# Performance work log

Hardware: AMD Instinct MI355X
Metric: run time of the kernel (lower is better)

Reference implementation:

```python
import jax, jax.numpy as jnp
import numpy as np

N = 50000      # nodes
D = 16         # regular in/out degree
E = N * D      # edges
IN_N = 128     # input node feature size
IN_E = 64      # input edge feature size
H = 64         # internal_size
H2 = 2 * H     # LSTM input/hidden size
OUT_N = 128
OUT_E = 64


def setup_inputs() -> dict:
    key = jax.random.key(0)
    ks = jax.random.split(key, 24)
    s = 0.05
    inp = {}
    inp["node_vecs"] = jax.random.normal(ks[0], (N, IN_N), jnp.float32)
    inp["edge_vecs"] = jax.random.normal(ks[1], (E, IN_E), jnp.float32)
    # ring digraph: edge e = i*D + k connects i -> (i+k+1) % N
    j = np.arange(N)[:, None]
    k = np.arange(D)[None, :]
    pni = (j - (k + 1)) % N
    inp["pred_node_idx"] = jnp.asarray(pni, jnp.int32)
    inp["pred_edge_idx"] = jnp.asarray(pni * D + k, jnp.int32)
    inp["succ_node_idx"] = jnp.asarray((j + k + 1) % N, jnp.int32)
    inp["succ_edge_idx"] = jnp.asarray(j * D + k, jnp.int32)
    src = np.repeat(np.arange(N), D)
    dst = (src + np.tile(np.arange(1, D + 1), N)) % N
    inp["edge_src"] = jnp.asarray(src, jnp.int32)
    inp["edge_dst"] = jnp.asarray(dst, jnp.int32)
    # parameters (torch Linear convention: y = x @ W.T + b)
    inp["Wn"] = jax.random.normal(ks[2], (H, IN_N), jnp.float32) * s
    inp["bn"] = jax.random.normal(ks[3], (H,), jnp.float32) * s
    inp["We"] = jax.random.normal(ks[4], (H, IN_E), jnp.float32) * s
    inp["be"] = jax.random.normal(ks[5], (H,), jnp.float32) * s
    # two LSTM aggregators (pred / succ), gate order i,f,g,o
    inp["Wih_p"] = jax.random.normal(ks[6], (4 * H2, H2), jnp.float32) * s
    inp["Whh_p"] = jax.random.normal(ks[7], (4 * H2, H2), jnp.float32) * s
    inp["bih_p"] = jax.random.normal(ks[8], (4 * H2,), jnp.float32) * s
    inp["bhh_p"] = jax.random.normal(ks[9], (4 * H2,), jnp.float32) * s
    inp["Wr_p"] = jax.random.normal(ks[10], (H, H2), jnp.float32) * s
    inp["br_p"] = jax.random.normal(ks[11], (H,), jnp.float32) * s
    inp["Wih_s"] = jax.random.normal(ks[12], (4 * H2, H2), jnp.float32) * s
    inp["Whh_s"] = jax.random.normal(ks[13], (4 * H2, H2), jnp.float32) * s
    inp["bih_s"] = jax.random.normal(ks[14], (4 * H2,), jnp.float32) * s
    inp["bhh_s"] = jax.random.normal(ks[15], (4 * H2,), jnp.float32) * s
    inp["Wr_s"] = jax.random.normal(ks[16], (H, H2), jnp.float32) * s
    inp["br_s"] = jax.random.normal(ks[17], (H,), jnp.float32) * s
    inp["Wt_n"] = jax.random.normal(ks[18], (OUT_N, 3 * H), jnp.float32) * s
    inp["bt_n"] = jax.random.normal(ks[19], (OUT_N,), jnp.float32) * s
    inp["Wt_e"] = jax.random.normal(ks[20], (OUT_E, 3 * H), jnp.float32) * s
    inp["bt_e"] = jax.random.normal(ks[21], (OUT_E,), jnp.float32) * s
    return inp


def _lstm_last(seq, Wih, Whh, bih, bhh):
    # seq: [N, D, 2H] -> last-timestep hidden state [N, 2H]
    n = seq.shape[0]
    h0 = jnp.zeros((n, H2), seq.dtype)

    def step(carry, x):
        h, c = carry
        g = x @ Wih.T + h @ Whh.T + (bih + bhh)
        i, f, gg, o = jnp.split(g, 4, axis=-1)
        c = jax.nn.sigmoid(f) * c + jax.nn.sigmoid(i) * jnp.tanh(gg)
        h = jax.nn.sigmoid(o) * jnp.tanh(c)
        return (h, c), None

    (h, _), _ = jax.lax.scan(step, (h0, h0), jnp.swapaxes(seq, 0, 1))
    return h


def _aggregate(hN, hE, nidx, eidx, Wih, Whh, bih, bhh, Wr, br):
    # gather neighbor sequences: concat(node pretrans, edge pretrans) -> [N, D, 2H]
    seq = jnp.concatenate([hN[nidx], hE[eidx]], axis=-1)
    h_last = _lstm_last(seq, Wih, Whh, bih, bhh)
    return jax.nn.relu(jax.nn.relu(h_last) @ Wr.T + br)  # [N, H]


def reference(node_vecs, edge_vecs, pred_node_idx, pred_edge_idx,
              succ_node_idx, succ_edge_idx, edge_src, edge_dst,
              Wn, bn, We, be,
              Wih_p, Whh_p, bih_p, bhh_p, Wr_p, br_p,
              Wih_s, Whh_s, bih_s, bhh_s, Wr_s, br_s,
              Wt_n, bt_n, Wt_e, bt_e):
    hN = jax.nn.relu(node_vecs @ Wn.T + bn)   # [N, H] node pretrans
    hE = jax.nn.relu(edge_vecs @ We.T + be)   # [E, H] edge pretrans
    agg_p = _aggregate(hN, hE, pred_node_idx, pred_edge_idx,
                       Wih_p, Whh_p, bih_p, bhh_p, Wr_p, br_p)
    agg_s = _aggregate(hN, hE, succ_node_idx, succ_edge_idx,
                       Wih_s, Whh_s, bih_s, bhh_s, Wr_s, br_s)
    node_in = jnp.concatenate([agg_p, hN, agg_s], axis=-1)      # [N, 3H]
    node_out = jax.nn.relu(node_in @ Wt_n.T + bt_n)             # [N, OUT_N]
    edge_in = jnp.concatenate([hN[edge_src], hE, hN[edge_dst]], axis=-1)  # [E, 3H]
    edge_out = jax.nn.relu(edge_in @ Wt_e.T + bt_e)             # [E, OUT_E]
    return node_out, edge_out
```

## Files before the change

### kernel.cpp

```cpp
#include <hip/hip_runtime.h>

#define DEV __device__ __forceinline__

typedef __bf16 bf16x8 __attribute__((ext_vector_type(8)));
typedef float floatx4 __attribute__((ext_vector_type(4)));
typedef unsigned short u16;

constexpr int NN    = 50000;
constexpr int DEG   = 16;
constexpr int H2    = 128;

constexpr size_t WS_WN    = 0;
constexpr size_t WS_WE    = 16384;
constexpr size_t WS_WIH_P = 24576;
constexpr size_t WS_WHH_P = 155648;
constexpr size_t WS_WR_P  = 286720;
constexpr size_t WS_WIH_S = 303104;
constexpr size_t WS_WHH_S = 434176;
constexpr size_t WS_WR_S  = 565248;
constexpr size_t WS_WT_N  = 581632;
constexpr size_t WS_WT_E  = 630784;
constexpr size_t WS_BSUM_P= 655360;
constexpr size_t WS_BSUM_S= 657408;
constexpr size_t WS_HN    = 659456;
constexpr size_t WS_AGGP  = 7059456;
constexpr size_t WS_AGGS  = 13459456;

DEV u16 f2bf(float x) {
  unsigned u = __builtin_bit_cast(unsigned, x);
  return (u16)((u + 0x7fffu + ((u >> 16) & 1u)) >> 16);
}
DEV bf16x8 ld8(const u16* p) { return *reinterpret_cast<const bf16x8*>(p); }
DEV floatx4 mfma16(bf16x8 a, bf16x8 b, floatx4 c) {
  return __builtin_amdgcn_mfma_f32_16x16x32_bf16(a, b, c, 0, 0, 0);
}
DEV floatx4 make4(float b) { floatx4 r = {b, b, b, b}; return r; }
DEV float sigf(float x) { return __builtin_amdgcn_rcpf(1.0f + __expf(-x)); }
DEV float expc(float x) { return __expf(fminf(x, 60.0f)); }
DEV bf16x8 relu8(bf16x8 a) {
  typedef u16 u16x8 __attribute__((ext_vector_type(8)));
  u16x8 u = __builtin_bit_cast(u16x8, a);
#pragma unroll
  for (int i = 0; i < 8; ++i) u[i] = (u[i] & 0x8000u) ? (u16)0 : u[i];
  return __builtin_bit_cast(bf16x8, u);
}

__global__ void k_prep(const float* Wn, const float* We,
                       const float* WihP, const float* WhhP, const float* WrP,
                       const float* WihS, const float* WhhS, const float* WrS,
                       const float* WtN, const float* WtE,
                       const float* bihP, const float* bhhP,
                       const float* bihS, const float* bhhS,
                       u16* wbf, float* bsumP, float* bsumS) {
  int idx = blockIdx.x * blockDim.x + threadIdx.x;
  if (idx < 327680) {
    const float* src; int rel;
    if      (idx <   8192) { src = Wn;   rel = idx; }
    else if (idx <  12288) { src = We;   rel = idx - 8192; }
    else if (idx <  77824) { src = WihP; rel = idx - 12288; }
    else if (idx < 143360) { src = WhhP; rel = idx - 77824; }
    else if (idx < 151552) { src = WrP;  rel = idx - 143360; }
    else if (idx < 217088) { src = WihS; rel = idx - 151552; }
    else if (idx < 282624) { src = WhhS; rel = idx - 217088; }
    else if (idx < 290816) { src = WrS;  rel = idx - 282624; }
    else if (idx < 315392) { src = WtN;  rel = idx - 290816; }
    else                   { src = WtE;  rel = idx - 315392; }
    wbf[idx] = f2bf(src[rel]);
  } else if (idx < 328704) {
    int j = idx - 327680;
    if (j < 512) bsumP[j] = bihP[j] + bhhP[j];
    else         bsumS[j - 512] = bihS[j - 512] + bhhS[j - 512];
  }
}

__global__ __launch_bounds__(256, 4) void k_pre_node(const float* xv, const float* bias,
                                                     const u16* Wbf, u16* outbf) {
  __shared__ __align__(16) u16 Xs[64 * 136];
  const int tid = threadIdx.x;
  const int base = blockIdx.x * 64;
#pragma unroll
  for (int j = 0; j < 8; ++j) {
    int flat = tid + j * 256;
    int row = flat >> 5, c4 = flat & 31;
    int gr = base + row; if (gr >= NN) gr = NN - 1;
    float4 v = reinterpret_cast<const float4*>(xv + (size_t)gr * 128)[c4];
    ushort4 h; h.x = f2bf(v.x); h.y = f2bf(v.y); h.z = f2bf(v.z); h.w = f2bf(v.w);
    *reinterpret_cast<ushort4*>(&Xs[row * 136 + c4 * 4]) = h;
  }
  __syncthreads();
  const int wave = tid >> 6, lane = tid & 63, l16 = lane & 15, quad = lane >> 4;
  const int rt = wave;
  floatx4 acc[4];
#pragma unroll
  for (int ct = 0; ct < 4; ++ct) acc[ct] = make4(bias[ct * 16 + l16]);
#pragma unroll
  for (int kt = 0; kt < 4; ++kt) {
    bf16x8 a = ld8(&Xs[(rt * 16 + l16) * 136 + kt * 32 + quad * 8]);
#pragma unroll
    for (int ct = 0; ct < 4; ++ct) {
      bf16x8 b = ld8(Wbf + (ct * 16 + l16) * 128 + kt * 32 + quad * 8);
      acc[ct] = mfma16(a, b, acc[ct]);
    }
  }
#pragma unroll
  for (int ct = 0; ct < 4; ++ct)
#pragma unroll
    for (int r = 0; r < 4; ++r) {
      int row = base + rt * 16 + quad * 4 + r;
      if (row < NN) {
        float v = acc[ct][r]; v = v > 0.0f ? v : 0.0f;
        outbf[(size_t)row * 64 + ct * 16 + l16] = f2bf(v);
      }
    }
}

__global__ __launch_bounds__(256, 4) void k_pre_edge(const float* xv, const float* bias,
                                                     const u16* Wbf, u16* outbf) {
  __shared__ __align__(16) u16 Xs[64 * 72];
  const int tid = threadIdx.x;
  const size_t base = (size_t)blockIdx.x * 64;
#pragma unroll
  for (int j = 0; j < 4; ++j) {
    int flat = tid + j * 256;
    int row = flat >> 4, c4 = flat & 15;
    float4 v = reinterpret_cast<const float4*>(xv + (base + row) * 64)[c4];
    ushort4 h; h.x = f2bf(v.x); h.y = f2bf(v.y); h.z = f2bf(v.z); h.w = f2bf(v.w);
    *reinterpret_cast<ushort4*>(&Xs[row * 72 + c4 * 4]) = h;
  }
  __syncthreads();
  const int wave = tid >> 6, lane = tid & 63, l16 = lane & 15, quad = lane >> 4;
  const int rt = wave;
  floatx4 acc[4];
#pragma unroll
  for (int ct = 0; ct < 4; ++ct) acc[ct] = make4(bias[ct * 16 + l16]);
#pragma unroll
  for (int kt = 0; kt < 2; ++kt) {
    bf16x8 a = ld8(&Xs[(rt * 16 + l16) * 72 + kt * 32 + quad * 8]);
#pragma unroll
    for (int ct = 0; ct < 4; ++ct) {
      bf16x8 b = ld8(Wbf + (ct * 16 + l16) * 64 + kt * 32 + quad * 8);
      acc[ct] = mfma16(a, b, acc[ct]);
    }
  }
#pragma unroll
  for (int ct = 0; ct < 4; ++ct)
#pragma unroll
    for (int r = 0; r < 4; ++r) {
      size_t row = base + rt * 16 + quad * 4 + r;
      float v = acc[ct][r]; v = v > 0.0f ? v : 0.0f;
      outbf[row * 128 + ct * 16 + l16] = f2bf(v);
    }
}

__global__ __launch_bounds__(512, 2) void k_lstm(
    const u16* hN, const u16* hE,
    const int* nidxP, const int* eidxP, const int* nidxS, const int* eidxS,
    const u16* WihP, const u16* WhhP, const float* bsumP, const u16* WrP, const float* brP, u16* aggP,
    const u16* WihS, const u16* WhhS, const float* bsumS, const u16* WrS, const float* brS, u16* aggS) {
  __shared__ __align__(16) u16 Xs[2][32 * 136];
  __shared__ __align__(16) u16 Hs[2][32 * 136];
  __shared__ int nidx_s[512], eidx_s[512];

  const bool s = (blockIdx.y != 0);
  const int* nidx = s ? nidxS : nidxP;
  const int* eidx = s ? eidxS : eidxP;
  const u16* Wih = s ? WihS : WihP;
  const u16* Whh = s ? WhhS : WhhP;
  const float* bsum = s ? bsumS : bsumP;
  const u16* Wr = s ? WrS : WrP;
  const float* br = s ? brS : brP;
  u16* aggOut = s ? aggS : aggP;

  const int tid = threadIdx.x;
  const int base = blockIdx.x * 32;
  {
    int g = base * 16 + tid;
    int vn = 0, ve = 0;
    if (g < NN * 16) { vn = nidx[g]; ve = eidx[g]; }
    nidx_s[tid] = vn; eidx_s[tid] = ve;
  }
  for (int j = tid; j < 32 * 136 / 2; j += 512) reinterpret_cast<unsigned*>(Hs[0])[j] = 0u;

  const int wave = tid >> 6, lane = tid & 63, l16 = lane & 15, quad = lane >> 4;

  bf16x8 wx[4][4], wh[4][4];
  float bias[4];
#pragma unroll
  for (int g = 0; g < 4; ++g) {
    int gc = g * 128 + wave * 16 + l16;
    bias[g] = bsum[gc];
#pragma unroll
    for (int kt = 0; kt < 4; ++kt) {
      wx[g][kt] = ld8(Wih + gc * 128 + kt * 32 + quad * 8);
      wh[g][kt] = ld8(Whh + gc * 128 + kt * 32 + quad * 8);
    }
  }
  floatx4 cst[2] = {make4(0.0f), make4(0.0f)};
  __syncthreads();

  const int srow = tid >> 4, sub = tid & 15, seg = sub >> 3, soff = (sub & 7) * 8;
  const u16* sbase = seg ? hE : hN;
  const size_t sstride = seg ? 128 : 64;
  const int* sidx = seg ? eidx_s : nidx_s;

  {
    int r0 = sidx[srow * 16];
    uint4 v0 = *reinterpret_cast<const uint4*>(sbase + (size_t)r0 * sstride + soff);
    *reinterpret_cast<uint4*>(&Xs[0][srow * 136 + seg * 64 + soff]) = v0;
  }
  __syncthreads();

  for (int t = 0; t < DEG; ++t) {
    const int cur = t & 1, nxt = cur ^ 1;
    int tn = (t + 1 < DEG) ? (t + 1) : t;
    int rn = sidx[srow * 16 + tn];
    uint4 vnext = *reinterpret_cast<const uint4*>(sbase + (size_t)rn * sstride + soff);

    floatx4 acc[4][2];
#pragma unroll
    for (int g = 0; g < 4; ++g) { acc[g][0] = make4(bias[g]); acc[g][1] = make4(bias[g]); }
    __builtin_amdgcn_s_setprio(1);
#pragma unroll
    for (int kt = 0; kt < 4; ++kt) {
      bf16x8 a0 = ld8(&Xs[cur][l16 * 136 + kt * 32 + quad * 8]);
#pragma unroll
      for (int g = 0; g < 4; ++g) acc[g][0] = mfma16(a0, wx[g][kt], acc[g][0]);
    }
#pragma unroll
    for (int kt = 0; kt < 4; ++kt) {
      bf16x8 h0 = ld8(&Hs[cur][l16 * 136 + kt * 32 + quad * 8]);
#pragma unroll
      for (int g = 0; g < 4; ++g) acc[g][0] = mfma16(h0, wh[g][kt], acc[g][0]);
    }
#pragma unroll
    for (int kt = 0; kt < 4; ++kt) {
      bf16x8 a1 = ld8(&Xs[cur][(16 + l16) * 136 + kt * 32 + quad * 8]);
#pragma unroll
      for (int g = 0; g < 4; ++g) acc[g][1] = mfma16(a1, wx[g][kt], acc[g][1]);
    }
#pragma unroll
    for (int kt = 0; kt < 4; ++kt) {
      bf16x8 h1 = ld8(&Hs[cur][(16 + l16) * 136 + kt * 32 + quad * 8]);
#pragma unroll
      for (int g = 0; g < 4; ++g) acc[g][1] = mfma16(h1, wh[g][kt], acc[g][1]);
    }
    __builtin_amdgcn_s_setprio(0);

#pragma unroll
    for (int hh = 0; hh < 2; ++hh) {
      float hv[4];
#pragma unroll
      for (int rr = 0; rr < 4; ++rr) {
        float gi = acc[0][hh][rr], gf = acc[1][hh][rr];
        float gg = acc[2][hh][rr], go = acc[3][hh][rr];
        float sf = sigf(gf);
        float ei = __expf(-gi);
        float eg = expc(-2.0f * gg);
        float r1 = __builtin_amdgcn_rcpf((1.0f + ei) * (1.0f + eg));
        float c  = __builtin_fmaf(sf, cst[hh][rr], (1.0f - eg) * r1);
        cst[hh][rr] = c;
        float eo = __expf(-go);
        float ec = expc(-2.0f * c);
        float r2 = __builtin_amdgcn_rcpf((1.0f + eo) * (1.0f + ec));
        hv[rr] = (1.0f - ec) * r2;
      }
#pragma unroll
      for (int rp = 0; rp < 2; ++rp) {
        unsigned pk;
        asm("v_cvt_pk_bf16_f32 %0, %1, %2" : "=v"(pk) : "v"(hv[rp * 2]), "v"(hv[rp * 2 + 1]));
        const int r0 = hh * 16 + quad * 4 + rp * 2;
        Hs[nxt][r0 * 136 + wave * 16 + l16] = (u16)pk;
        Hs[nxt][(r0 + 1) * 136 + wave * 16 + l16] = (u16)(pk >> 16);
      }
    }

    if (t + 1 < DEG)
      *reinterpret_cast<uint4*>(&Xs[nxt][srow * 136 + seg * 64 + soff]) = vnext;
    __syncthreads();
  }

  {
    const int rt = wave >> 2, ct = wave & 3;
    floatx4 acc = make4(br[ct * 16 + l16]);
#pragma unroll
    for (int kt = 0; kt < 4; ++kt) {
      bf16x8 a = relu8(ld8(&Hs[0][(rt * 16 + l16) * 136 + kt * 32 + quad * 8]));
      bf16x8 b = ld8(Wr + (ct * 16 + l16) * 128 + kt * 32 + quad * 8);
      acc = mfma16(a, b, acc);
    }
#pragma unroll
    for (int rr = 0; rr < 4; ++rr) {
      int row = base + rt * 16 + quad * 4 + rr;
      if (row < NN) {
        float v = acc[rr] > 0.0f ? acc[rr] : 0.0f;
        aggOut[(size_t)row * 64 + ct * 16 + l16] = f2bf(v);
      }
    }
  }
}

__global__ __launch_bounds__(256, 4) void k_node_out(
    const u16* aggP, const u16* hN, const u16* aggS,
    const u16* Wt, const float* bt, float* outp) {
  __shared__ __align__(16) u16 Xs[64 * 200];
  const int tid = threadIdx.x;
  const int base = blockIdx.x * 64;
  const u16* segp[3] = {aggP, hN, aggS};
#pragma unroll
  for (int seg = 0; seg < 3; ++seg)
#pragma unroll
    for (int j = 0; j < 2; ++j) {
      int flat = tid + j * 256;
      int row = flat >> 3, off = (flat & 7) * 8;
      int gr = base + row; if (gr >= NN) gr = NN - 1;
      uint4 v = *reinterpret_cast<const uint4*>(segp[seg] + (size_t)gr * 64 + off);
      *reinterpret_cast<uint4*>(&Xs[row * 200 + seg * 64 + off]) = v;
    }
  __syncthreads();
  const int wave = tid >> 6, lane = tid & 63, l16 = lane & 15, quad = lane >> 4;
  const int rt = wave;
  floatx4 acc[8];
#pragma unroll
  for (int ct = 0; ct < 8; ++ct) acc[ct] = make4(bt[ct * 16 + l16]);
#pragma unroll
  for (int kt = 0; kt < 6; ++kt) {
    bf16x8 a = ld8(&Xs[(rt * 16 + l16) * 200 + kt * 32 + quad * 8]);
#pragma unroll
    for (int ct = 0; ct < 8; ++ct) {
      bf16x8 b = ld8(Wt + (ct * 16 + l16) * 192 + kt * 32 + quad * 8);
      acc[ct] = mfma16(a, b, acc[ct]);
    }
  }
#pragma unroll
  for (int ct = 0; ct < 8; ++ct)
#pragma unroll
    for (int r = 0; r < 4; ++r) {
      int row = base + rt * 16 + quad * 4 + r;
      if (row < NN) {
        float v = acc[ct][r];
        __builtin_nontemporal_store(v > 0.0f ? v : 0.0f,
                                    &outp[(size_t)row * 128 + ct * 16 + l16]);
      }
    }
}

__global__ __launch_bounds__(256, 4) void k_edge_out(
    const u16* hN, const u16* hE, const int* esrc, const int* edst,
    const u16* Wt, const float* bt, float* outp) {
  __shared__ __align__(16) u16 Xs[64 * 200];
  __shared__ int idxs[128];
  const int tid = threadIdx.x;
  const size_t base = (size_t)blockIdx.x * 64;
  if (tid < 64) idxs[tid] = esrc[base + tid];
  else if (tid < 128) idxs[tid] = edst[base + tid - 64];
  __syncthreads();
#pragma unroll
  for (int seg = 0; seg < 3; ++seg)
#pragma unroll
    for (int j = 0; j < 2; ++j) {
      int flat = tid + j * 256;
      int row = flat >> 3, off = (flat & 7) * 8;
      size_t grow;
      const u16* sp;
      if (seg == 0)      { grow = (size_t)idxs[row] * 64;       sp = hN; }
      else if (seg == 1) { grow = (base + row) * 128;           sp = hE; }
      else               { grow = (size_t)idxs[64 + row] * 64;  sp = hN; }
      uint4 v = *reinterpret_cast<const uint4*>(sp + grow + off);
      *reinterpret_cast<uint4*>(&Xs[row * 200 + seg * 64 + off]) = v;
    }
  __syncthreads();
  const int wave = tid >> 6, lane = tid & 63, l16 = lane & 15, quad = lane >> 4;
  const int rt = wave;
  floatx4 acc[4];
#pragma unroll
  for (int ct = 0; ct < 4; ++ct) acc[ct] = make4(bt[ct * 16 + l16]);
#pragma unroll
  for (int kt = 0; kt < 6; ++kt) {
    bf16x8 a = ld8(&Xs[(rt * 16 + l16) * 200 + kt * 32 + quad * 8]);
#pragma unroll
    for (int ct = 0; ct < 4; ++ct) {
      bf16x8 b = ld8(Wt + (ct * 16 + l16) * 192 + kt * 32 + quad * 8);
      acc[ct] = mfma16(a, b, acc[ct]);
    }
  }
#pragma unroll
  for (int ct = 0; ct < 4; ++ct)
#pragma unroll
    for (int r = 0; r < 4; ++r) {
      size_t row = base + rt * 16 + quad * 4 + r;
      float v = acc[ct][r];
      __builtin_nontemporal_store(v > 0.0f ? v : 0.0f,
                                  &outp[row * 64 + ct * 16 + l16]);
    }
}

extern "C" void kernel_launch(void* const* d_in, const int* in_sizes, int n_in,
                              void* d_out, int out_size, void* d_ws, size_t ws_size,
                              hipStream_t stream) {
  (void)in_sizes; (void)n_in; (void)out_size; (void)ws_size;
  const float* node_vecs = (const float*)d_in[0];
  const float* edge_vecs = (const float*)d_in[1];
  const int* pred_node_idx = (const int*)d_in[2];
  const int* pred_edge_idx = (const int*)d_in[3];
  const int* succ_node_idx = (const int*)d_in[4];
  const int* succ_edge_idx = (const int*)d_in[5];
  const int* edge_src = (const int*)d_in[6];
  const int* edge_dst = (const int*)d_in[7];
  const float* Wn = (const float*)d_in[8];
  const float* bn = (const float*)d_in[9];
  const float* We = (const float*)d_in[10];
  const float* be = (const float*)d_in[11];
  const float* Wih_p = (const float*)d_in[12];
  const float* Whh_p = (const float*)d_in[13];
  const float* bih_p = (const float*)d_in[14];
  const float* bhh_p = (const float*)d_in[15];
  const float* Wr_p = (const float*)d_in[16];
  const float* br_p = (const float*)d_in[17];
  const float* Wih_s = (const float*)d_in[18];
  const float* Whh_s = (const float*)d_in[19];
  const float* bih_s = (const float*)d_in[20];
  const float* bhh_s = (const float*)d_in[21];
  const float* Wr_s = (const float*)d_in[22];
  const float* br_s = (const float*)d_in[23];
  const float* Wt_n = (const float*)d_in[24];
  const float* bt_n = (const float*)d_in[25];
  const float* Wt_e = (const float*)d_in[26];
  const float* bt_e = (const float*)d_in[27];

  char* ws = (char*)d_ws;
  u16* wWn   = (u16*)(ws + WS_WN);
  u16* wWe   = (u16*)(ws + WS_WE);
  u16* wWihP = (u16*)(ws + WS_WIH_P);
  u16* wWhhP = (u16*)(ws + WS_WHH_P);
  u16* wWrP  = (u16*)(ws + WS_WR_P);
  u16* wWihS = (u16*)(ws + WS_WIH_S);
  u16* wWhhS = (u16*)(ws + WS_WHH_S);
  u16* wWrS  = (u16*)(ws + WS_WR_S);
  u16* wWtN  = (u16*)(ws + WS_WT_N);
  u16* wWtE  = (u16*)(ws + WS_WT_E);
  float* bsumP = (float*)(ws + WS_BSUM_P);
  float* bsumS = (float*)(ws + WS_BSUM_S);
  u16* hN   = (u16*)(ws + WS_HN);
  u16* aggP = (u16*)(ws + WS_AGGP);
  u16* aggS = (u16*)(ws + WS_AGGS);
  float* outN = (float*)d_out;
  float* outE = outN + (size_t)NN * 128;
  u16* hE = (u16*)outE;

  k_prep<<<1284, 256, 0, stream>>>(Wn, We, Wih_p, Whh_p, Wr_p, Wih_s, Whh_s, Wr_s,
                                   Wt_n, Wt_e, bih_p, bhh_p, bih_s, bhh_s,
                                   (u16*)ws, bsumP, bsumS);
  k_pre_node<<<782, 256, 0, stream>>>(node_vecs, bn, wWn, hN);
  k_pre_edge<<<12500, 256, 0, stream>>>(edge_vecs, be, wWe, hE);
  dim3 g3(1563, 2, 1);
  k_lstm<<<g3, 512, 0, stream>>>(hN, hE,
                                 pred_node_idx, pred_edge_idx, succ_node_idx, succ_edge_idx,
                                 wWihP, wWhhP, bsumP, wWrP, br_p, aggP,
                                 wWihS, wWhhS, bsumS, wWrS, br_s, aggS);
  k_node_out<<<782, 256, 0, stream>>>(aggP, hN, aggS, wWtN, bt_n, outN);
  k_edge_out<<<12500, 256, 0, stream>>>(hN, hE, edge_src, edge_dst, wWtE, bt_e, outE);
}
```

Measured before the change: 1.153 ms.

## Stage pretrans outputs via LDS for coalesced stores; prefetch LSTM inputs two steps ahead

The node and edge pretrans kernels now write their relu outputs into shared memory and then store them to global memory as 16-byte coalesced chunks, instead of scattered 2-byte stores. The LSTM gather is deepened from one-step to two-step register prefetch so each step's global load has more time to land. The s_setprio hints around the MFMA block are removed. In exchange the change adds an extra barrier and LDS pass in the pretrans kernels and more live registers in the LSTM kernel.

```diff
diff --git a/kernel.cpp b/kernel.cpp
--- a/kernel.cpp
+++ b/kernel.cpp
@@ -106,12 +106,20 @@
   for (int ct = 0; ct < 4; ++ct)
 #pragma unroll
     for (int r = 0; r < 4; ++r) {
-      int row = base + rt * 16 + quad * 4 + r;
-      if (row < NN) {
-        float v = acc[ct][r]; v = v > 0.0f ? v : 0.0f;
-        outbf[(size_t)row * 64 + ct * 16 + l16] = f2bf(v);
-      }
-    }
+      float v = acc[ct][r]; v = v > 0.0f ? v : 0.0f;
+      Xs[(rt * 16 + quad * 4 + r) * 136 + ct * 16 + l16] = f2bf(v);
+    }
+  __syncthreads();
+#pragma unroll
+  for (int j = 0; j < 2; ++j) {
+    int ch = tid + j * 256;
+    int row = ch >> 3, off8 = (ch & 7) * 8;
+    int gr = base + row;
+    if (gr < NN) {
+      uint4 v = *reinterpret_cast<const uint4*>(&Xs[row * 136 + off8]);
+      *reinterpret_cast<uint4*>(outbf + (size_t)gr * 64 + off8) = v;
+    }
+  }
 }
 
 __global__ __launch_bounds__(256, 4) void k_pre_edge(const float* xv, const float* bias,
@@ -146,10 +154,17 @@
   for (int ct = 0; ct < 4; ++ct)
 #pragma unroll
     for (int r = 0; r < 4; ++r) {
-      size_t row = base + rt * 16 + quad * 4 + r;
       float v = acc[ct][r]; v = v > 0.0f ? v : 0.0f;
-      outbf[row * 128 + ct * 16 + l16] = f2bf(v);
-    }
+      Xs[(rt * 16 + quad * 4 + r) * 72 + ct * 16 + l16] = f2bf(v);
+    }
+  __syncthreads();
+#pragma unroll
+  for (int j = 0; j < 2; ++j) {
+    int ch = tid + j * 256;
+    int row = ch >> 3, off8 = (ch & 7) * 8;
+    uint4 v = *reinterpret_cast<const uint4*>(&Xs[row * 72 + off8]);
+    *reinterpret_cast<uint4*>(outbf + (base + row) * 128 + off8) = v;
+  }
 }
 
 __global__ __launch_bounds__(512, 2) void k_lstm(
@@ -208,18 +223,22 @@
     uint4 v0 = *reinterpret_cast<const uint4*>(sbase + (size_t)r0 * sstride + soff);
     *reinterpret_cast<uint4*>(&Xs[0][srow * 136 + seg * 64 + soff]) = v0;
   }
+  uint4 vA;
+  {
+    int r1 = sidx[srow * 16 + 1];
+    vA = *reinterpret_cast<const uint4*>(sbase + (size_t)r1 * sstride + soff);
+  }
   __syncthreads();
 
   for (int t = 0; t < DEG; ++t) {
     const int cur = t & 1, nxt = cur ^ 1;
-    int tn = (t + 1 < DEG) ? (t + 1) : t;
+    int tn = (t + 2 < DEG) ? (t + 2) : (DEG - 1);
     int rn = sidx[srow * 16 + tn];
-    uint4 vnext = *reinterpret_cast<const uint4*>(sbase + (size_t)rn * sstride + soff);
+    uint4 vB = *reinterpret_cast<const uint4*>(sbase + (size_t)rn * sstride + soff);
 
     floatx4 acc[4][2];
 #pragma unroll
     for (int g = 0; g < 4; ++g) { acc[g][0] = make4(bias[g]); acc[g][1] = make4(bias[g]); }
-    __builtin_amdgcn_s_setprio(1);
 #pragma unroll
     for (int kt = 0; kt < 4; ++kt) {
       bf16x8 a0 = ld8(&Xs[cur][l16 * 136 + kt * 32 + quad * 8]);
@@ -244,7 +263,6 @@
 #pragma unroll
       for (int g = 0; g < 4; ++g) acc[g][1] = mfma16(h1, wh[g][kt], acc[g][1]);
     }
-    __builtin_amdgcn_s_setprio(0);
 
 #pragma unroll
     for (int hh = 0; hh < 2; ++hh) {
@@ -275,7 +293,8 @@
     }
 
     if (t + 1 < DEG)
-      *reinterpret_cast<uint4*>(&Xs[nxt][srow * 136 + seg * 64 + soff]) = vnext;
+      *reinterpret_cast<uint4*>(&Xs[nxt][srow * 136 + seg * 64 + soff]) = vA;
+    vA = vB;
     __syncthreads();
   }
 
```

New measurement: 1.118 ms. 1.03x faster.
